# Kernel optimization log

Measured on AMD Instinct MI355X. Metric: run time of the kernel, lower is better.

Reference implementation:

```python
import jax, jax.numpy as jnp
import numpy as np

D = 256   # koopman_dim
B = 256   # batch of initial latent states
T_STEPS = 512
DT = 0.01


def setup_inputs() -> dict:
    key = jax.random.key(0)
    k1, k2 = jax.random.split(key)
    z0 = jax.random.normal(k1, (B, D), dtype=jnp.float32)
    # nnx.Linear default lecun_normal init: std ~ 1/sqrt(fan_in)
    kernel = jax.random.normal(k2, (D, D), dtype=jnp.float32) / jnp.sqrt(jnp.float32(D))
    log_dt = jnp.asarray(jnp.log(DT), dtype=jnp.float32)
    return {"z0": z0, "kernel": kernel, "log_dt": log_dt, "T": T_STEPS}


def reference(z0, kernel, log_dt, T):
    dt = jnp.exp(log_dt)
    eye = jnp.eye(kernel.shape[0], dtype=kernel.dtype)
    # Bilinear / Tustin discretization: K_d = (I - 0.5*dt*K)^-1 (I + 0.5*dt*K)
    K_discrete = jnp.linalg.solve(eye - 0.5 * dt * kernel, eye + 0.5 * dt * kernel)

    def step(z, _):
        z_next = z @ K_discrete  # [B, D] @ [D, D]
        return z_next, z_next

    _, preds = jax.lax.scan(step, z0, None, length=T)  # preds: [T, B, D]
    return jnp.transpose(preds, (1, 0, 2))  # [B, T, D]
```

## Files before the change

kernel.cpp:

```cpp
#include <hip/hip_runtime.h>


#define DD 256
#define TT 512
#define MATF (DD * DD)
#define LDT ((size_t)TT * (size_t)DD)

typedef __attribute__((ext_vector_type(8))) short bf16x8;
typedef __attribute__((ext_vector_type(4))) float f32x4;

#define GLD16(g, l)                                                  \
    __builtin_amdgcn_global_load_lds(                                \
        (const __attribute__((address_space(1))) void*)(g),          \
        (__attribute__((address_space(3))) void*)(l), 16, 0, 0)

static __device__ __forceinline__ unsigned short f2bf(float f) {
    unsigned int u = __float_as_uint(f);
    u += 0x7fffu + ((u >> 16) & 1u);
    return (unsigned short)(u >> 16);
}
static __device__ __forceinline__ unsigned pack2bf(float a, float b) {
    return (unsigned)f2bf(a) | ((unsigned)f2bf(b) << 16);
}

__device__ __forceinline__ void g32_core(const float* __restrict__ Ab, int lda,
                                         const float* __restrict__ Bb, int ldb,
                                         int rowBase, int colBase, float acc[2][2]) {
    __shared__ __align__(16) float As[64 * 38];
    __shared__ __align__(16) float Bs[64 * 40];
    const int tid = threadIdx.x;
    const int tx = tid & 15, ty = tid >> 4;
    const int am = tid >> 4;
    const int ak = (tid & 15) << 2;
    const int bk = tid >> 3;
    const int bn = (tid & 7) << 2;

    acc[0][0] = acc[0][1] = acc[1][0] = acc[1][1] = 0.f;

    float4 pa0 = *(const float4*)(Ab + (size_t)(rowBase + am) * lda + ak);
    float4 pa1 = *(const float4*)(Ab + (size_t)(rowBase + am + 16) * lda + ak);
    float4 pb0 = *(const float4*)(Bb + (size_t)bk * ldb + colBase + bn);
    float4 pb1 = *(const float4*)(Bb + (size_t)(bk + 32) * ldb + colBase + bn);

    for (int k0 = 0; k0 < DD; k0 += 64) {
        As[(ak + 0) * 38 + am] = pa0.x;
        As[(ak + 1) * 38 + am] = pa0.y;
        As[(ak + 2) * 38 + am] = pa0.z;
        As[(ak + 3) * 38 + am] = pa0.w;
        As[(ak + 0) * 38 + am + 16] = pa1.x;
        As[(ak + 1) * 38 + am + 16] = pa1.y;
        As[(ak + 2) * 38 + am + 16] = pa1.z;
        As[(ak + 3) * 38 + am + 16] = pa1.w;
        *(float4*)(&Bs[bk * 40 + bn]) = pb0;
        *(float4*)(&Bs[(bk + 32) * 40 + bn]) = pb1;
        __syncthreads();
        if (k0 + 64 < DD) {
            pa0 = *(const float4*)(Ab + (size_t)(rowBase + am) * lda + k0 + 64 + ak);
            pa1 = *(const float4*)(Ab + (size_t)(rowBase + am + 16) * lda + k0 + 64 + ak);
            pb0 = *(const float4*)(Bb + (size_t)(bk + k0 + 64) * ldb + colBase + bn);
            pb1 = *(const float4*)(Bb + (size_t)(bk + 32 + k0 + 64) * ldb + colBase + bn);
        }
#pragma unroll
        for (int kk = 0; kk < 64; ++kk) {
            float2 a2 = *(const float2*)(&As[kk * 38 + (ty << 1)]);
            float2 b2 = *(const float2*)(&Bs[kk * 40 + (tx << 1)]);
            acc[0][0] = fmaf(a2.x, b2.x, acc[0][0]);
            acc[0][1] = fmaf(a2.x, b2.y, acc[0][1]);
            acc[1][0] = fmaf(a2.y, b2.x, acc[1][0]);
            acc[1][1] = fmaf(a2.y, b2.y, acc[1][1]);
        }
        __syncthreads();
    }
}

__global__ void __launch_bounds__(256)
n1_kernel(const float* __restrict__ K, const float* __restrict__ log_dt,
          const float* __restrict__ z0, float* __restrict__ A2,
          float* __restrict__ Bop, unsigned short* __restrict__ Zb0) {
    const float cs = 0.5f * expf(log_dt[0]);
    {
        int b = ((blockIdx.y * 8 + blockIdx.x) * 256 + threadIdx.x) * 4;
        uint2 w;
        w.x = pack2bf(z0[b], z0[b + 1]);
        w.y = pack2bf(z0[b + 2], z0[b + 3]);
        *(uint2*)(Zb0 + b) = w;
    }
    float acc[2][2];
    const int rowBase = blockIdx.y << 5, colBase = blockIdx.x << 5;
    g32_core(K, DD, K, DD, rowBase, colBase, acc);
    const float cs2 = cs * cs;
    const int r0 = rowBase + ((threadIdx.x >> 4) << 1);
    const int c0 = colBase + ((threadIdx.x & 15) << 1);
#pragma unroll
    for (int i = 0; i < 2; ++i) {
        int r = r0 + i;
        float e0 = K[(size_t)r * DD + c0], e1 = K[(size_t)r * DD + c0 + 1];
        float p0 = cs2 * acc[i][0], p1 = cs2 * acc[i][1];
        *(float2*)(A2 + (size_t)r * DD + c0) = (float2){p0, p1};
        float2 w;
        w.x = 2.f * p0 + 2.f * cs * e0 + (r == c0 ? 2.f : 0.f);
        w.y = 2.f * p1 + 2.f * cs * e1 + (r == c0 + 1 ? 2.f : 0.f);
        *(float2*)(Bop + (size_t)r * DD + c0) = w;
    }
}

__global__ void __launch_bounds__(256)
n2_kernel(const float* __restrict__ A2, const float* __restrict__ Bop,
          const float* __restrict__ K, const float* __restrict__ log_dt,
          float* __restrict__ E) {
    const float cs = 0.5f * expf(log_dt[0]);
    float acc[2][2];
    const int rowBase = blockIdx.y << 5, colBase = blockIdx.x << 5;
    g32_core(A2, DD, Bop, DD, rowBase, colBase, acc);
    const int r0 = rowBase + ((threadIdx.x >> 4) << 1);
    const int c0 = colBase + ((threadIdx.x & 15) << 1);
#pragma unroll
    for (int i = 0; i < 2; ++i) {
        int r = r0 + i;
        float e0 = K[(size_t)r * DD + c0], e1 = K[(size_t)r * DD + c0 + 1];
        float2 v;
        v.x = acc[i][0] + 2.f * cs * e0;
        v.y = acc[i][1] + 2.f * cs * e1;
        *(float2*)(E + (size_t)r * DD + c0) = v;
    }
}

__global__ void __launch_bounds__(256)
gpow_kernel(const float* __restrict__ A, const float* __restrict__ B,
            float* __restrict__ C, long long sA, long long sB, long long sC) {
    float acc[2][2];
    const int rowBase = blockIdx.y << 5, colBase = blockIdx.x << 5;
    g32_core(A + blockIdx.z * sA, DD, B + blockIdx.z * sB, DD, rowBase, colBase, acc);
    float* Cb = C + blockIdx.z * sC;
    const int r0 = rowBase + ((threadIdx.x >> 4) << 1);
    const int c0 = colBase + ((threadIdx.x & 15) << 1);
#pragma unroll
    for (int i = 0; i < 2; ++i) {
        int r = r0 + i;
        *(float2*)(Cb + (size_t)r * DD + c0) = (float2){acc[i][0], acc[i][1]};
    }
}

__global__ void __launch_bounds__(256)
gpow4_kernel(float* __restrict__ Epow) {
    static const int sa[4] = {1, 2, 2, 3};
    static const int sb[4] = {2, 2, 3, 3};
    static const int sc[4] = {4, 5, 6, 7};
    const int z = blockIdx.z;
    float acc[2][2];
    const int rowBase = blockIdx.y << 5, colBase = blockIdx.x << 5;
    g32_core(Epow + (size_t)sa[z] * MATF, DD, Epow + (size_t)sb[z] * MATF, DD,
             rowBase, colBase, acc);
    float* Cb = Epow + (size_t)sc[z] * MATF;
    const int r0 = rowBase + ((threadIdx.x >> 4) << 1);
    const int c0 = colBase + ((threadIdx.x & 15) << 1);
#pragma unroll
    for (int i = 0; i < 2; ++i) {
        int r = r0 + i;
        *(float2*)(Cb + (size_t)r * DD + c0) = (float2){acc[i][0], acc[i][1]};
    }
}

__global__ void __launch_bounds__(256)
comb_kernel(const float* __restrict__ Epow, unsigned short* __restrict__ MTb,
            float* __restrict__ W1, float* __restrict__ W2,
            float* __restrict__ W3) {
    __shared__ float tle[8][32][33];
    const int tid = threadIdx.x;
    const int k0 = blockIdx.y << 5, c0 = blockIdx.x << 5;
    const int ltx = tid & 31, lty = tid >> 5;
#pragma unroll
    for (int m = 0; m < 8; ++m)
#pragma unroll
        for (int it = 0; it < 4; ++it) {
            int k = lty + (it << 3);
            tle[m][ltx][k] =
                Epow[(size_t)m * MATF + (size_t)(k0 + k) * DD + c0 + ltx];
        }
    __syncthreads();

    const int c = tid >> 3;
    const int kb = (tid & 7) << 2;
    float em[8][4];
#pragma unroll
    for (int m = 0; m < 8; ++m)
#pragma unroll
        for (int u = 0; u < 4; ++u) em[m][u] = tle[m][c][kb + u];

    float diag[4];
#pragma unroll
    for (int u = 0; u < 4; ++u)
        diag[u] = ((k0 + kb + u) == (c0 + c)) ? 1.f : 0.f;

    float w32[4];
    for (int j = 1; j <= 32; ++j) {
        float val[4] = {diag[0], diag[1], diag[2], diag[3]};
        long long coef = 1;
#pragma unroll
        for (int m = 1; m <= 8; ++m) {
            coef = coef * (j - m + 1) / m;
            float cf = (float)(coef < 0 ? 0 : coef);
#pragma unroll
            for (int u = 0; u < 4; ++u) val[u] = fmaf(cf, em[m - 1][u], val[u]);
        }
        uint2 w;
        w.x = pack2bf(val[0], val[1]);
        w.y = pack2bf(val[2], val[3]);
        *(uint2*)(MTb + (size_t)(j - 1) * MATF + (size_t)(c0 + c) * DD + k0 + kb) = w;
        if (j == 32) {
            w32[0] = val[0]; w32[1] = val[1]; w32[2] = val[2]; w32[3] = val[3];
        }
    }
    float w64[4] = {diag[0], diag[1], diag[2], diag[3]};
    float w96[4] = {diag[0], diag[1], diag[2], diag[3]};
    {
        double c64 = 1.0, c96 = 1.0;
#pragma unroll
        for (int m = 1; m <= 8; ++m) {
            c64 = c64 * (double)(64 - m + 1) / (double)m;
            c96 = c96 * (double)(96 - m + 1) / (double)m;
            float f64 = (float)c64, f96 = (float)c96;
#pragma unroll
            for (int u = 0; u < 4; ++u) {
                w64[u] = fmaf(f64, em[m - 1][u], w64[u]);
                w96[u] = fmaf(f96, em[m - 1][u], w96[u]);
            }
        }
    }
    float* tw = &tle[0][0][0];
    const int wk = tid >> 3, wc = (tid & 7) << 2;
    float* Wd[3] = {W1, W2, W3};
    float* Ws[3] = {w32, w64, w96};
#pragma unroll
    for (int p = 0; p < 3; ++p) {
        __syncthreads();
#pragma unroll
        for (int u = 0; u < 4; ++u) tw[(kb + u) * 33 + c] = Ws[p][u];
        __syncthreads();
        float4 v = {tw[wk * 33 + wc], tw[wk * 33 + wc + 1],
                    tw[wk * 33 + wc + 2], tw[wk * 33 + wc + 3]};
        *(float4*)(Wd[p] + (size_t)(k0 + wk) * DD + c0 + wc) = v;
    }
}

__global__ void __launch_bounds__(256)
scan3_kernel(const float* __restrict__ z0, float* __restrict__ out,
             const float* __restrict__ W1, const float* __restrict__ W2,
             const float* __restrict__ W3, float* __restrict__ Wtab,
             unsigned short* __restrict__ Zb, int level) {
    static const signed char JA[3][7] = {{0, 0, 0, 17, 18, 0, 0},
                                         {0, 1, 2, 3, 2, 3, 20},
                                         {4, 5, 0, 1, 2, 3, 0}};
    static const signed char JB[3][7] = {{0, 1, 2, 1, 2, 0, 0},
                                         {3, 3, 3, 3, 4, 4, 4},
                                         {4, 4, 5, 5, 5, 5, 0}};
    static const signed char JD[3][7] = {{1, 2, 3, 19, 20, 0, 0},
                                         {4, 5, 6, 7, 8, 9, 21},
                                         {10, 11, 12, 13, 14, 15, 0}};
    const float* Wp[6] = {W1, W2, W3, Wtab, Wtab + MATF, Wtab + 2 * (size_t)MATF};
    const int jz = blockIdx.z;
    const int a = JA[level][jz], b = JB[level][jz], d = JD[level][jz];

    const float* Asrc;
    int lda;
    if (a == 0) { Asrc = z0; lda = DD; }
    else if (a < 16) { Asrc = out + (size_t)(32 * a - 1) * DD; lda = (int)LDT; }
    else { Asrc = Wp[a - 16]; lda = DD; }

    float acc[2][2];
    const int rowBase = blockIdx.y << 5, colBase = blockIdx.x << 5;
    g32_core(Asrc, lda, Wp[b], DD, rowBase, colBase, acc);

    const int r0 = rowBase + ((threadIdx.x >> 4) << 1);
    const int c0 = colBase + ((threadIdx.x & 15) << 1);
    if (d < 16) {
        float* Of = out + (size_t)(32 * d - 1) * DD;
        unsigned short* Zo = Zb + (size_t)d * MATF;
#pragma unroll
        for (int ii = 0; ii < 2; ++ii) {
            int r = r0 + ii;
            float2 v = {acc[ii][0], acc[ii][1]};
            *(float2*)(Of + (size_t)r * LDT + c0) = v;
            *(unsigned*)(Zo + (size_t)r * DD + c0) = pack2bf(v.x, v.y);
        }
    } else {
        float* Cb = Wtab + (size_t)(d - 19) * MATF;
#pragma unroll
        for (int ii = 0; ii < 2; ++ii) {
            int r = r0 + ii;
            *(float2*)(Cb + (size_t)r * DD + c0) = (float2){acc[ii][0], acc[ii][1]};
        }
    }
}

__global__ void __launch_bounds__(256)
fill_kernel(const unsigned short* __restrict__ Zb,
            const unsigned short* __restrict__ MTb,
            float* __restrict__ out) {
    __shared__ __align__(16) char pool[32768];
    const int bz = blockIdx.z;
    const int i = (bz >= 465) ? 15 : bz / 31;
    const int j = bz - i * 31 + 1;
    const int t = i * 32 + j - 1;
    const unsigned short* Zt = Zb + (size_t)i * MATF;
    const unsigned short* MT = MTb + (size_t)(j - 1) * MATF;

    const int tid = threadIdx.x;
    const int lane = tid & 63, wid = tid >> 6;
    const int rowBase = blockIdx.y * 128, colBase = blockIdx.x * 128;
    const int wr = (wid >> 1) * 64, wc = (wid & 1) * 64;

    int rowq[4], skq[4], ldsb[4];
#pragma unroll
    for (int q = 0; q < 4; ++q) {
        int c = q * 256 + wid * 64 + lane;
        int row = c >> 3;
        rowq[q] = row;
        skq[q] = ((c ^ (row & 7)) & 7) << 3;
        ldsb[q] = (q * 256 + wid * 64) << 4;
    }

    f32x4 acc[4][4];
#pragma unroll
    for (int a = 0; a < 4; ++a)
#pragma unroll
        for (int b = 0; b < 4; ++b) acc[a][b] = (f32x4){0.f, 0.f, 0.f, 0.f};

    auto stage = [&](int k0) {
#pragma unroll
        for (int q = 0; q < 4; ++q) {
            GLD16(Zt + (size_t)(rowBase + rowq[q]) * DD + k0 + skq[q], pool + ldsb[q]);
            GLD16(MT + (size_t)(colBase + rowq[q]) * DD + k0 + skq[q],
                  pool + 16384 + ldsb[q]);
        }
    };

    stage(0);
    for (int r = 0; r < 4; ++r) {
        __syncthreads();
        const char* asb = pool;
        const char* bsb = pool + 16384;
#pragma unroll
        for (int ks = 0; ks < 2; ++ks) {
            bf16x8 af[4], bg[4];
            const int kk = ks * 32 + (lane >> 4) * 8;
#pragma unroll
            for (int f = 0; f < 4; ++f) {
                int rr = wr + f * 16 + (lane & 15);
                af[f] = *(const bf16x8*)(asb + ((rr * 128 + kk * 2) ^ ((rr & 7) << 4)));
                int cc = wc + f * 16 + (lane & 15);
                bg[f] = *(const bf16x8*)(bsb + ((cc * 128 + kk * 2) ^ ((cc & 7) << 4)));
            }
#pragma unroll
            for (int fr = 0; fr < 4; ++fr)
#pragma unroll
                for (int fc = 0; fc < 4; ++fc)
                    acc[fr][fc] = __builtin_amdgcn_mfma_f32_16x16x32_bf16(
                        af[fr], bg[fc], acc[fr][fc], 0, 0, 0);
        }
        __syncthreads();
        if (r < 3) stage((r + 1) * 64);
    }

    float* Cs = (float*)pool;
    float* C = out + (size_t)t * DD;
#pragma unroll
    for (int hp = 0; hp < 2; ++hp) {
        __syncthreads();
        if (wr == hp * 64) {
#pragma unroll
            for (int fr = 0; fr < 4; ++fr) {
#pragma unroll
                for (int fc = 0; fc < 4; ++fc) {
                    int ccol = wc + fc * 16 + (lane & 15);
#pragma unroll
                    for (int ii = 0; ii < 4; ++ii) {
                        int lr = fr * 16 + ((lane >> 4) << 2) + ii;
                        int csw = ccol ^ (((lr >> 2) & 1) << 4);
                        Cs[lr * 128 + csw] = acc[fr][fc][ii];
                    }
                }
            }
        }
        __syncthreads();
#pragma unroll
        for (int it = 0; it < 8; ++it) {
            int chunk = it * 256 + tid;
            int row = chunk >> 5;
            int c4 = (chunk & 31) << 2;
            int csw = c4 ^ (((row >> 2) & 1) << 4);
            float4 v = *(const float4*)(Cs + row * 128 + csw);
            *(float4*)(C + (size_t)(rowBase + hp * 64 + row) * LDT + colBase + c4) = v;
        }
    }
}

__global__ void prep_kernel(const float* __restrict__ K,
                            const float* __restrict__ log_dt,
                            float* __restrict__ A) {
    int idx = blockIdx.x * blockDim.x + threadIdx.x;
    A[idx] = 0.5f * expf(log_dt[0]) * K[idx];
}

template <int EPI>
__global__ void __launch_bounds__(256)
g32_kernel(const float* A, const float* B, float* C, const float* E, float* C2,
           int lda, int ldb, int ldc, long long sA, long long sB, long long sC) {
    float acc[2][2];
    const int rowBase = blockIdx.y << 5, colBase = blockIdx.x << 5;
    g32_core(A + blockIdx.z * sA, lda, B + blockIdx.z * sB, ldb, rowBase, colBase, acc);
    float* Cb = C + blockIdx.z * sC;
    const int r0 = rowBase + ((threadIdx.x >> 4) << 1);
    const int c0 = colBase + ((threadIdx.x & 15) << 1);
#pragma unroll
    for (int i = 0; i < 2; ++i) {
        int r = r0 + i;
        float2 v;
        if (EPI == 2) {
            float e0 = E[(size_t)r * DD + c0], e1 = E[(size_t)r * DD + c0 + 1];
            v.x = acc[i][0] + 2.f * e0 + (r == c0 ? 1.f : 0.f);
            v.y = acc[i][1] + 2.f * e1 + (r == c0 + 1 ? 1.f : 0.f);
        } else {
            v.x = acc[i][0];
            v.y = acc[i][1];
        }
        *(float2*)(Cb + (size_t)r * ldc + c0) = v;
        if (EPI == 1) {
            float e0 = E[(size_t)r * DD + c0], e1 = E[(size_t)r * DD + c0 + 1];
            float2 w;
            w.x = 2.f * acc[i][0] + 2.f * e0 + (r == c0 ? 2.f : 0.f);
            w.y = 2.f * acc[i][1] + 2.f * e1 + (r == c0 + 1 ? 2.f : 0.f);
            *(float2*)(C2 + (size_t)r * DD + c0) = w;
        }
    }
}

extern "C" void kernel_launch(void* const* d_in, const int* in_sizes, int n_in,
                              void* d_out, int out_size, void* d_ws, size_t ws_size,
                              hipStream_t stream) {
    const float* z0 = (const float*)d_in[0];
    const float* Kmat = (const float*)d_in[1];
    const float* log_dt = (const float*)d_in[2];
    float* out = (float*)d_out;

    dim3 blk(256);

    float* A2 = (float*)d_ws;
    float* Bop = A2 + MATF;
    float* Epow = Bop + MATF;
    float* W1 = Epow + (size_t)8 * MATF;
    float* W2 = W1 + MATF;
    float* W3 = W2 + MATF;
    float* Wtab = W3 + MATF;
    unsigned short* MTb = (unsigned short*)(Wtab + (size_t)3 * MATF);
    unsigned short* Zb = MTb + (size_t)32 * MATF;
    const size_t need = (size_t)16 * MATF * 4 + (size_t)48 * MATF * 2;

    if (ws_size >= need) {
        dim3 g(8, 8, 1);
        n1_kernel<<<g, blk, 0, stream>>>(Kmat, log_dt, z0, A2, Bop, Zb);
        n2_kernel<<<g, blk, 0, stream>>>(A2, Bop, Kmat, log_dt, Epow);

        gpow_kernel<<<g, blk, 0, stream>>>(Epow, Epow, Epow + MATF, 0, 0, 0);
        gpow_kernel<<<dim3(8, 8, 2), blk, 0, stream>>>(
            Epow, Epow + MATF, Epow + 2 * (size_t)MATF, MATF, 0, MATF);
        gpow4_kernel<<<dim3(8, 8, 4), blk, 0, stream>>>(Epow);

        comb_kernel<<<g, blk, 0, stream>>>(Epow, MTb, W1, W2, W3);

        const int njobs[3] = {5, 7, 6};
        for (int s = 0; s < 3; ++s)
            scan3_kernel<<<dim3(8, 8, njobs[s]), blk, 0, stream>>>(
                z0, out, W1, W2, W3, Wtab, Zb, s);

        fill_kernel<<<dim3(2, 2, 497), blk, 0, stream>>>(Zb, MTb, out);
        return;
    }

    float* A = (float*)d_ws;
    float* A2f = A + MATF;
    float* Bopf = A2f + MATF;
    float* Kd = Bopf + MATF;
    prep_kernel<<<MATF / 256, blk, 0, stream>>>(Kmat, log_dt, A);
    dim3 g(8, 8, 1);
    g32_kernel<1><<<g, blk, 0, stream>>>(A, A, A2f, A, Bopf, DD, DD, DD, 0, 0, 0);
    g32_kernel<2><<<g, blk, 0, stream>>>(A2f, Bopf, Kd, A, (float*)0, DD, DD, DD, 0, 0, 0);
    for (int t = 0; t < TT; ++t) {
        const float* Ain = (t == 0) ? z0 : out + (size_t)(t - 1) * DD;
        int lda = (t == 0) ? DD : (int)LDT;
        g32_kernel<0><<<g, blk, 0, stream>>>(Ain, Kd, out + (size_t)t * DD,
                                             (const float*)0, (float*)0,
                                             lda, DD, (int)LDT, 0, 0, 0);
    }
}
```

Before: 120.0 us.

## Compute full 256x256 output per block in fill kernel with 512 threads

Each fill_kernel block now computes the whole 256x256 product for one time step with 8 waves, instead of four 128x128 tiles spread over separate blocks. This loads each Z and M^T k-slice once per step rather than twice, and cuts the grid to 497 blocks. In exchange, the cross-iteration prefetch of the next k-slice is dropped, so loads no longer overlap MFMA work. LDS rises to 64KB per block and the 128 accumulator floats per thread may pressure registers and occupancy.

```diff
diff --git a/kernel.cpp b/kernel.cpp
--- a/kernel.cpp
+++ b/kernel.cpp
@@ -293,12 +293,12 @@
     }
 }
 
-__global__ void __launch_bounds__(256)
+__global__ void __launch_bounds__(512, 2)
 fill_kernel(const unsigned short* __restrict__ Zb,
             const unsigned short* __restrict__ MTb,
             float* __restrict__ out) {
-    __shared__ __align__(16) char pool[32768];
-    const int bz = blockIdx.z;
+    __shared__ __align__(16) char pool[65536];
+    const int bz = blockIdx.x;
     const int i = (bz >= 465) ? 15 : bz / 31;
     const int j = bz - i * 31 + 1;
     const int t = i * 32 + j - 1;
@@ -307,77 +307,78 @@
 
     const int tid = threadIdx.x;
     const int lane = tid & 63, wid = tid >> 6;
-    const int rowBase = blockIdx.y * 128, colBase = blockIdx.x * 128;
-    const int wr = (wid >> 1) * 64, wc = (wid & 1) * 64;
+    const int wr = (wid >> 2) * 128, wc = (wid & 3) * 64;
 
     int rowq[4], skq[4], ldsb[4];
 #pragma unroll
     for (int q = 0; q < 4; ++q) {
-        int c = q * 256 + wid * 64 + lane;
+        int c = q * 512 + wid * 64 + lane;
         int row = c >> 3;
         rowq[q] = row;
-        skq[q] = ((c ^ (row & 7)) & 7) << 3;
-        ldsb[q] = (q * 256 + wid * 64) << 4;
-    }
-
-    f32x4 acc[4][4];
-#pragma unroll
-    for (int a = 0; a < 4; ++a)
+        skq[q] = ((c ^ row) & 7) << 3;
+        ldsb[q] = (q * 512 + wid * 64) << 4;
+    }
+
+    f32x4 acc[8][4];
+#pragma unroll
+    for (int a = 0; a < 8; ++a)
 #pragma unroll
         for (int b = 0; b < 4; ++b) acc[a][b] = (f32x4){0.f, 0.f, 0.f, 0.f};
 
     auto stage = [&](int k0) {
 #pragma unroll
         for (int q = 0; q < 4; ++q) {
-            GLD16(Zt + (size_t)(rowBase + rowq[q]) * DD + k0 + skq[q], pool + ldsb[q]);
-            GLD16(MT + (size_t)(colBase + rowq[q]) * DD + k0 + skq[q],
-                  pool + 16384 + ldsb[q]);
+            GLD16(Zt + (size_t)rowq[q] * DD + k0 + skq[q], pool + ldsb[q]);
+            GLD16(MT + (size_t)rowq[q] * DD + k0 + skq[q], pool + 32768 + ldsb[q]);
         }
     };
 
-    stage(0);
     for (int r = 0; r < 4; ++r) {
+        stage(r * 64);
         __syncthreads();
         const char* asb = pool;
-        const char* bsb = pool + 16384;
+        const char* bsb = pool + 32768;
 #pragma unroll
         for (int ks = 0; ks < 2; ++ks) {
-            bf16x8 af[4], bg[4];
+            bf16x8 af[8], bg[4];
             const int kk = ks * 32 + (lane >> 4) * 8;
 #pragma unroll
-            for (int f = 0; f < 4; ++f) {
+            for (int f = 0; f < 8; ++f) {
                 int rr = wr + f * 16 + (lane & 15);
                 af[f] = *(const bf16x8*)(asb + ((rr * 128 + kk * 2) ^ ((rr & 7) << 4)));
+            }
+#pragma unroll
+            for (int f = 0; f < 4; ++f) {
                 int cc = wc + f * 16 + (lane & 15);
                 bg[f] = *(const bf16x8*)(bsb + ((cc * 128 + kk * 2) ^ ((cc & 7) << 4)));
             }
 #pragma unroll
-            for (int fr = 0; fr < 4; ++fr)
+            for (int fr = 0; fr < 8; ++fr)
 #pragma unroll
                 for (int fc = 0; fc < 4; ++fc)
                     acc[fr][fc] = __builtin_amdgcn_mfma_f32_16x16x32_bf16(
                         af[fr], bg[fc], acc[fr][fc], 0, 0, 0);
         }
         __syncthreads();
-        if (r < 3) stage((r + 1) * 64);
     }
 
     float* Cs = (float*)pool;
     float* C = out + (size_t)t * DD;
 #pragma unroll
-    for (int hp = 0; hp < 2; ++hp) {
-        __syncthreads();
-        if (wr == hp * 64) {
-#pragma unroll
-            for (int fr = 0; fr < 4; ++fr) {
+    for (int hp = 0; hp < 4; ++hp) {
+        __syncthreads();
+        if ((wid >> 2) == (hp >> 1)) {
+            const int fbase = (hp & 1) * 4;
+#pragma unroll
+            for (int f = 0; f < 4; ++f) {
 #pragma unroll
                 for (int fc = 0; fc < 4; ++fc) {
                     int ccol = wc + fc * 16 + (lane & 15);
 #pragma unroll
                     for (int ii = 0; ii < 4; ++ii) {
-                        int lr = fr * 16 + ((lane >> 4) << 2) + ii;
-                        int csw = ccol ^ (((lr >> 2) & 1) << 4);
-                        Cs[lr * 128 + csw] = acc[fr][fc][ii];
+                        int lr = f * 16 + ((lane >> 4) << 2) + ii;
+                        int csw = ccol ^ (((lr >> 2) & 3) << 4);
+                        Cs[lr * 256 + csw] = acc[fbase + f][fc][ii];
                     }
                 }
             }
@@ -385,12 +386,12 @@
         __syncthreads();
 #pragma unroll
         for (int it = 0; it < 8; ++it) {
-            int chunk = it * 256 + tid;
-            int row = chunk >> 5;
-            int c4 = (chunk & 31) << 2;
-            int csw = c4 ^ (((row >> 2) & 1) << 4);
-            float4 v = *(const float4*)(Cs + row * 128 + csw);
-            *(float4*)(C + (size_t)(rowBase + hp * 64 + row) * LDT + colBase + c4) = v;
+            int chunk = it * 512 + tid;
+            int row = chunk >> 6;
+            int c4 = (chunk & 63) << 2;
+            int csw = c4 ^ (((row >> 2) & 3) << 4);
+            float4 v = *(const float4*)(Cs + row * 256 + csw);
+            *(float4*)(C + (size_t)(hp * 64 + row) * LDT + c4) = v;
         }
     }
 }
@@ -473,7 +474,7 @@
             scan3_kernel<<<dim3(8, 8, njobs[s]), blk, 0, stream>>>(
                 z0, out, W1, W2, W3, Wtab, Zb, s);
 
-        fill_kernel<<<dim3(2, 2, 497), blk, 0, stream>>>(Zb, MTb, out);
+        fill_kernel<<<dim3(497), dim3(512), 0, stream>>>(Zb, MTb, out);
         return;
     }
 
```

After: 124.9 us. 4.0% more time.
